# Kernel optimization log

Measured on AMD Instinct MI355X. Metric: run time of the kernel, lower is better.

## Reference

```python
import jax, jax.numpy as jnp
import numpy as np

H = 400      # LSTM hidden units
K = 10       # attention window mixture components (mixtures=30 -> alpha/beta/kappa of size K)
V = 61       # vocab_size
NOUT = 121   # MDN head: 1 eos + 20*(pi, mu1, mu2, sigma1, sigma2, rho)


def setup_inputs():
    key = jax.random.key(0)
    ks = jax.random.split(key, 12)
    B, T, U = 32, 600, 64
    s = 0.05
    d = {}
    d['strokes'] = jax.random.normal(ks[0], (B, T, 3), jnp.float32)
    d['sentence'] = jax.random.uniform(ks[1], (B, U, V), dtype=jnp.float32)
    d['W1'] = jax.random.normal(ks[2], (3 + V, 4 * H), jnp.float32) * s
    d['U1r'] = jax.random.normal(ks[3], (H, 4 * H), jnp.float32) * s
    d['b1'] = jnp.zeros((4 * H,), jnp.float32)
    d['Ww'] = jax.random.normal(ks[4], (H, 3 * K), jnp.float32) * s
    d['bw'] = jnp.zeros((3 * K,), jnp.float32)
    d['W2'] = jax.random.normal(ks[5], (3 + V + H, 4 * H), jnp.float32) * s
    d['U2r'] = jax.random.normal(ks[6], (H, 4 * H), jnp.float32) * s
    d['b2'] = jnp.zeros((4 * H,), jnp.float32)
    d['W3'] = jax.random.normal(ks[7], (3 + V + H, 4 * H), jnp.float32) * s
    d['U3r'] = jax.random.normal(ks[8], (H, 4 * H), jnp.float32) * s
    d['b3'] = jnp.zeros((4 * H,), jnp.float32)
    d['Wm'] = jax.random.normal(ks[9], (3 * H, NOUT), jnp.float32) * s
    d['bm'] = jnp.zeros((NOUT,), jnp.float32)
    return d


def _lstm(x_tbd, W, Ur, b, h0, c0):
    # standard Keras-order (i, f, g, o) LSTM over time-major input [T,B,D]
    def step(carry, xt):
        h, c = carry
        z = xt @ W + h @ Ur + b
        i, f, g, o = jnp.split(z, 4, axis=-1)
        c = jax.nn.sigmoid(f) * c + jax.nn.sigmoid(i) * jnp.tanh(g)
        h = jax.nn.sigmoid(o) * jnp.tanh(c)
        return (h, c), h
    _, hs = jax.lax.scan(step, (h0, c0), x_tbd)
    return hs


def _forward(strokes, sentence, W1, U1r, b1, Ww, bw, W2, U2r, b2, W3, U3r, b3, Wm, bm):
    B, T, _ = strokes.shape
    U = sentence.shape[1]
    u_grid = jnp.arange(U, dtype=strokes.dtype)           # character positions
    x_tb = jnp.transpose(strokes, (1, 0, 2))               # [T,B,3]
    h0 = jnp.zeros((B, H), strokes.dtype)
    w0 = jnp.zeros((B, V), strokes.dtype)
    k0 = jnp.zeros((B, K), strokes.dtype)

    def step1(carry, xt):
        # Graves synthesis windowed LSTM cell: LSTM on [x_t, w_{t-1}],
        # then Gaussian-mixture soft attention over the sentence.
        h, c, w, kappa = carry
        xin = jnp.concatenate([xt, w], axis=-1)            # [B, 3+V]
        z = xin @ W1 + h @ U1r + b1
        i, f, g, o = jnp.split(z, 4, axis=-1)
        c = jax.nn.sigmoid(f) * c + jax.nn.sigmoid(i) * jnp.tanh(g)
        h = jax.nn.sigmoid(o) * jnp.tanh(c)
        p = h @ Ww + bw                                    # [B, 3K]
        alpha = jnp.exp(p[:, :K])
        beta = jnp.exp(p[:, K:2 * K])
        kappa = kappa + jnp.exp(p[:, 2 * K:])
        # phi(u) = sum_k alpha_k exp(-beta_k (kappa_k - u)^2)  -> [B,U]
        phi = jnp.einsum('bk,bku->bu', alpha,
                         jnp.exp(-beta[:, :, None] * (kappa[:, :, None] - u_grid) ** 2))
        w = jnp.einsum('bu,buv->bv', phi, sentence)        # soft window [B,V]
        return (h, c, w, kappa), jnp.concatenate([h, w], axis=-1)

    _, o1 = jax.lax.scan(step1, (h0, h0, w0, k0), x_tb)    # [T,B,H+V]
    lstm1 = o1[:, :, :H]
    win = o1[:, :, H:]
    in2 = jnp.concatenate([x_tb, win, lstm1], axis=-1)     # skip1: [T,B,3+V+H]
    lstm2 = _lstm(in2, W2, U2r, b2, h0, h0)
    in3 = jnp.concatenate([x_tb, win, lstm2], axis=-1)     # skip2
    lstm3 = _lstm(in3, W3, U3r, b3, h0, h0)
    y = jnp.concatenate([lstm1, lstm2, lstm3], axis=-1) @ Wm + bm  # [T,B,121]
    # MDN mixture coefficients
    e = jax.nn.sigmoid(y[..., 0:1])
    pi = jax.nn.softmax(y[..., 1:21], axis=-1)
    mu1 = y[..., 21:41]
    mu2 = y[..., 41:61]
    s1 = jnp.exp(y[..., 61:81])
    s2 = jnp.exp(y[..., 81:101])
    rho = jnp.tanh(y[..., 101:121])
    out = jnp.concatenate([e, pi, mu1, mu2, s1, s2, rho], axis=-1)
    return jnp.transpose(out, (1, 0, 2))                   # [B,T,121]


def reference(strokes, sentence, W1, U1r, b1, Ww, bw, W2, U2r, b2, W3, U3r, b3, Wm, bm):
    return _forward(strokes, sentence, W1, U1r, b1, Ww, bw, W2, U2r, b2, W3, U3r, b3, Wm, bm)
```

## Files before the change

kernel.cpp:

```cpp
#include <hip/hip_runtime.h>
#include <math.h>

#define T 600
#define NBLK 235

#define SEN1 256
#define SEN2 1536
#define SEN3 3072
#define SENB 4608

#define OFF_UT1 8192
#define SZ_UT1 (1600*480)
#define OFF_UT2 (OFF_UT1 + SZ_UT1)
#define SZ_UT2 (1600*960)
#define OFF_UT3 (OFF_UT2 + SZ_UT2)
#define OFF_WWT (OFF_UT3 + SZ_UT2)
#define SZ_WWT (30*400)
#define OFF_H1 (OFF_WWT + SZ_WWT)
#define SZ_H (600*32*400)
#define OFF_H2 (OFF_H1 + SZ_H)
#define OFF_H3 (OFF_H2 + SZ_H)
#define OFF_W  (OFF_H3 + SZ_H)
#define SZ_W (600*32*61)

#define LDS_W    0
#define LDS_V    19280
#define LDS_Z    34640
#define LDS_C    35408
#define LDS_TOT  35600

__device__ __forceinline__ float sigm(float x) { return 1.f/(1.f+expf(-x)); }

#define WBAR() do { \
    asm volatile("s_waitcnt lgkmcnt(0)" ::: "memory"); \
    __builtin_amdgcn_sched_barrier(0); \
} while (0)

__global__ void init_ws(unsigned* uws) {
    for (int i = threadIdx.x + blockIdx.x*blockDim.x; i < 8192; i += blockDim.x*gridDim.x)
        uws[i] = 0u;
}

__global__ void build_ut(float* __restrict__ ws,
                         const float* __restrict__ W1, const float* __restrict__ U1r,
                         const float* __restrict__ W2, const float* __restrict__ U2r,
                         const float* __restrict__ W3, const float* __restrict__ U3r,
                         const float* __restrict__ Ww) {
    const long N1 = 1600L*480, N2 = 1600L*960;
    const long total = N1 + 2*N2 + 30L*400;
    for (long i = blockIdx.x*(long)blockDim.x + threadIdx.x; i < total;
         i += (long)gridDim.x*blockDim.x) {
        if (i < N1) {
            long c = i / 480, k = i % 480;
            float v = 0.f;
            if (k < 64) v = W1[k*1600 + c];
            else if (k < 464) v = U1r[(k-64)*1600 + c];
            ws[OFF_UT1 + c*480 + k] = v;
        } else if (i < N1 + N2) {
            long ii = i - N1; long c = ii/960, k = ii%960;
            float v = 0.f;
            if (k < 464) v = W2[k*1600 + c];
            else if (k >= 480 && k < 880) v = U2r[(k-480)*1600 + c];
            ws[OFF_UT2 + c*960 + k] = v;
        } else if (i < N1 + 2*N2) {
            long ii = i - N1 - N2; long c = ii/960, k = ii%960;
            float v = 0.f;
            if (k < 464) v = W3[k*1600 + c];
            else if (k >= 480 && k < 880) v = U3r[(k-480)*1600 + c];
            ws[OFF_UT3 + c*960 + k] = v;
        } else {
            long ii = i - N1 - 2*N2; long n = ii/400, k = ii%400;
            ws[OFF_WWT + n*400 + k] = Ww[k*30 + n];
        }
    }
}

__device__ __forceinline__ unsigned ld_cohere(const unsigned* p) {
    unsigned v;
    asm volatile("global_load_dword %0, %1, off sc0 sc1\n\t"
                 "s_waitcnt vmcnt(0)"
                 : "=v"(v) : "v"(p) : "memory");
    return v;
}
__device__ __forceinline__ void st_wt(float* p, float v) {
    asm volatile("global_store_dword %0, %1, off sc0 sc1\n\t"
                 "s_waitcnt vmcnt(0)"
                 :: "v"(p), "v"(v) : "memory");
}
__device__ __forceinline__ void st_wt_u(unsigned* p, unsigned v) {
    asm volatile("global_store_dword %0, %1, off sc0 sc1\n\t"
                 "s_waitcnt vmcnt(0)"
                 :: "v"(p), "v"(v) : "memory");
}
__device__ __forceinline__ void wait_sen(const unsigned* sen, int count,
                                         unsigned tgt, int tid) {
    if (tid < 64) {
        for (;;) {
            unsigned m = 0xFFFFFFFFu;
            for (int i = tid; i < count; i += 64) {
                unsigned v = ld_cohere(sen + (size_t)i*16);
                m = (v < m) ? v : m;
            }
            if (__all(m >= tgt)) break;
            __builtin_amdgcn_s_sleep(1);
        }
    }
    __syncthreads();
}

template<int NQ, int KCN, int K4S, int LO, int HI>
__device__ __forceinline__ void gemm_pass(const float4* __restrict__ w4,
                                          const float4* __restrict__ v4,
                                          int lc0, int kc, int bq, int kofs4,
                                          float acc[8][4]) {
    #pragma unroll
    for (int q = 0; q < NQ; ++q) {
        int kfv = q*KCN + kc;
        if (kfv >= LO && kfv < HI) {
            int xv = kfv ^ ((kfv >> 3) & 7);
            int kfw = kofs4 + kfv;
            int xw = kfw ^ ((kfw >> 3) & 7);
            float4 va[8];
            #pragma unroll
            for (int i = 0; i < 8; ++i) va[i] = v4[(bq*8+i)*120 + xv];
            #pragma unroll
            for (int j = 0; j < 4; ++j) {
                float4 u = w4[(lc0+j)*K4S + xw];
                #pragma unroll
                for (int i = 0; i < 8; ++i)
                    acc[i][j] += va[i].x*u.x + va[i].y*u.y + va[i].z*u.z + va[i].w*u.w;
            }
        }
    }
}

__launch_bounds__(512)
__global__ void hw_main(float* __restrict__ ws,
                        const float* __restrict__ strokes, const float* __restrict__ sentence,
                        const float* __restrict__ b1, const float* __restrict__ b2,
                        const float* __restrict__ b3, const float* __restrict__ bw) {
    extern __shared__ float S[];
    const int tid = threadIdx.x;
    const int bid = blockIdx.x;
    unsigned* uws = (unsigned*)ws;
    const unsigned* sen1 = uws + SEN1;
    const unsigned* sen2 = uws + SEN2;
    const unsigned* sen3 = uws + SEN3;
    const unsigned* senB = uws + SENB;

    int role, unit0 = 0, nu = 0, L = 0, b0a = 0;
    const float* utp = nullptr; const float* biasp = nullptr; float* hout = nullptr;
    if (bid < 67)       { role = 0; L = bid;      unit0 = L*6; nu = (bid==66)?4:6; utp = ws+OFF_UT1; biasp = b1; hout = ws+OFF_H1; }
    else if (bid < 147) { role = 1; L = bid-67;   unit0 = L*5; nu = 5;             utp = ws+OFF_UT2; biasp = b2; hout = ws+OFF_H2; }
    else if (bid < 227) { role = 2; L = bid-147;  unit0 = L*5; nu = 5;             utp = ws+OFF_UT3; biasp = b3; hout = ws+OFF_H3; }
    else                { role = 3; L = bid-227;  b0a = L*4; }

    if (role <= 2) {
        const int NC = 4*nu;
        const int KCN = (role == 0) ? 20 : 24;
        const int K4S = (role == 0) ? 121 : 241;
        const int K4TOT = (role == 0) ? 120 : 240;
        const int uts = (role == 0) ? 480 : 960;
        float4* w4 = (float4*)S;
        float4* v4 = (float4*)(S + LDS_V);
        float*  vf = S + LDS_V;
        float*  z_lds = S + LDS_Z;
        float*  c_lds = S + LDS_C;

        for (int idx = tid; idx < NC*K4TOT; idx += 512) {
            int colL = idx / K4TOT, kf = idx % K4TOT;
            int gcol = (colL/nu)*400 + unit0 + (colL%nu);
            float4 val = *(const float4*)(utp + (size_t)gcol*uts + kf*4);
            w4[colL*K4S + (kf ^ ((kf>>3)&7))] = val;
        }
        for (int i = tid; i < 192; i += 512) c_lds[i] = 0.f;

        const int tile = tid / KCN, kc = tid % KCN;
        const int bq = tile / nu, cq = tile % nu;
        const bool act = (tile < 4*nu);
        float bias0 = 0.f, bias1 = 0.f;
        if (tid < 32*NC)       { int lc = tid % NC;        bias0 = biasp[(lc/nu)*400 + unit0 + (lc%nu)]; }
        if (tid + 512 < 32*NC) { int lc = (tid+512) % NC;  bias1 = biasp[(lc/nu)*400 + unit0 + (lc%nu)]; }
        const int nrole = (role == 0) ? 67 : 80;
        const unsigned* mysen = (role == 0) ? sen1 : ((role == 1) ? sen2 : sen3);
        unsigned* myword = (unsigned*)mysen + (size_t)L*16;
        __syncthreads();

        for (int t = 0; t < T; ++t) {
            float acc[8][4];
            #pragma unroll
            for (int i = 0; i < 8; ++i)
                #pragma unroll
                for (int j = 0; j < 4; ++j) acc[i][j] = 0.f;

            if (role == 0) {
                if (t > 0) wait_sen(sen1, 67, (unsigned)t, tid);
                const float* hsrc = (t > 0) ? (ws + OFF_H1 + (size_t)(t-1)*12800) : nullptr;
                for (int idx = tid; idx < 32*104; idx += 512) {
                    int b = idx/104, kf = 16 + idx%104;
                    float4 val = {0.f,0.f,0.f,0.f};
                    if (kf < 116 && hsrc) val = *(const float4*)(hsrc + b*400 + (kf*4 - 64));
                    v4[b*120 + (kf ^ ((kf>>3)&7))] = val;
                }
                __syncthreads();
                if (act) gemm_pass<6,20,121,16,116>(w4, v4, cq*4, kc, bq, 0, acc);
                if (t > 0) wait_sen(senB, 8, (unsigned)t, tid);
                const float* wsrc = (t > 0) ? (ws + OFF_W + (size_t)(t-1)*1952) : nullptr;
                {
                    int b = tid / 16, kf = tid % 16;
                    if (b < 32) {
                        float4 val;
                        if (kf == 0) {
                            const float* xp = strokes + ((size_t)b*600 + t)*3;
                            val.x = xp[0]; val.y = xp[1]; val.z = xp[2];
                            val.w = wsrc ? wsrc[b*61] : 0.f;
                        } else {
                            int k0 = kf*4 - 3;
                            if (wsrc) { val.x = wsrc[b*61+k0]; val.y = wsrc[b*61+k0+1];
                                        val.z = wsrc[b*61+k0+2]; val.w = wsrc[b*61+k0+3]; }
                            else { val.x=val.y=val.z=val.w=0.f; }
                        }
                        v4[b*120 + (kf ^ ((kf>>3)&7))] = val;
                    }
                }
                __syncthreads();
                if (act) gemm_pass<6,20,121,0,16>(w4, v4, cq*4, kc, bq, 0, acc);
            } else {
                if (role == 1) wait_sen(sen1, 67, (unsigned)(t+1), tid);
                else           wait_sen(sen2, 80, (unsigned)(t+1), tid);
                const float* hsrc = ws + ((role==1)?OFF_H1:OFF_H2) + (size_t)t*12800;
                for (int idx = tid; idx < 32*104; idx += 512) {
                    int b = idx/104, kf = 16 + idx%104;
                    float4 val = {0.f,0.f,0.f,0.f};
                    if (kf < 116) val = *(const float4*)(hsrc + b*400 + (kf*4 - 64));
                    v4[b*120 + (kf ^ ((kf>>3)&7))] = val;
                }
                __syncthreads();
                if (act) gemm_pass<5,24,241,16,116>(w4, v4, cq*4, kc, bq, 0, acc);
                wait_sen(senB, 8, (unsigned)(t+1), tid);
                const float* wsrc = ws + OFF_W + (size_t)t*1952;
                {
                    int b = tid / 16, kf = tid % 16;
                    if (b < 32) {
                        float4 val;
                        if (kf == 0) {
                            const float* xp = strokes + ((size_t)b*600 + t)*3;
                            val.x = xp[0]; val.y = xp[1]; val.z = xp[2];
                            val.w = wsrc[b*61];
                        } else {
                            int k0 = kf*4 - 3;
                            val.x = wsrc[b*61+k0]; val.y = wsrc[b*61+k0+1];
                            val.z = wsrc[b*61+k0+2]; val.w = wsrc[b*61+k0+3];
                        }
                        v4[b*120 + (kf ^ ((kf>>3)&7))] = val;
                    }
                }
                __syncthreads();
                if (act) gemm_pass<5,24,241,0,16>(w4, v4, cq*4, kc, bq, 0, acc);
                __syncthreads();
                if (t > 0) wait_sen(mysen, nrole, (unsigned)t, tid);
                const float* hp2 = (t > 0) ? (ws + ((role==1)?OFF_H2:OFF_H3) + (size_t)(t-1)*12800) : nullptr;
                for (int idx = tid; idx < 32*120; idx += 512) {
                    int b = idx/120, kf = idx%120;
                    float4 val = {0.f,0.f,0.f,0.f};
                    if (kf < 100 && hp2) val = *(const float4*)(hp2 + b*400 + kf*4);
                    v4[b*120 + (kf ^ ((kf>>3)&7))] = val;
                }
                __syncthreads();
                if (act) gemm_pass<5,24,241,0,100>(w4, v4, cq*4, kc, bq, 120, acc);
            }

            __syncthreads();
            const int halfk = (KCN+1)/2;
            const int SCRW = NC*32 + 4;
            const int NO = 32*NC;
            if (act && kc < halfk) {
                #pragma unroll
                for (int i = 0; i < 8; ++i) {
                    float4 w;
                    w.x=acc[i][0]; w.y=acc[i][1]; w.z=acc[i][2]; w.w=acc[i][3];
                    *(float4*)&vf[kc*SCRW + (bq*8+i)*NC + cq*4] = w;
                }
            }
            __syncthreads();
            float zs0 = 0.f, zs1 = 0.f;
            if (tid < NO)       for (int k2 = 0; k2 < halfk; ++k2) zs0 += vf[k2*SCRW + tid];
            if (tid + 512 < NO) for (int k2 = 0; k2 < halfk; ++k2) zs1 += vf[k2*SCRW + tid + 512];
            __syncthreads();
            if (act && kc >= halfk) {
                #pragma unroll
                for (int i = 0; i < 8; ++i) {
                    float4 w;
                    w.x=acc[i][0]; w.y=acc[i][1]; w.z=acc[i][2]; w.w=acc[i][3];
                    *(float4*)&vf[(kc-halfk)*SCRW + (bq*8+i)*NC + cq*4] = w;
                }
            }
            __syncthreads();
            const int rem = KCN - halfk;
            if (tid < NO) {
                for (int k2 = 0; k2 < rem; ++k2) zs0 += vf[k2*SCRW + tid];
                z_lds[tid] = zs0 + bias0;
            }
            if (tid + 512 < NO) {
                for (int k2 = 0; k2 < rem; ++k2) zs1 += vf[k2*SCRW + tid + 512];
                z_lds[tid + 512] = zs1 + bias1;
            }
            __syncthreads();
            if (tid < 32*nu) {
                int b = tid & 31, ju = tid >> 5;
                float zi = z_lds[b*NC + ju];
                float zf = z_lds[b*NC + nu + ju];
                float zg = z_lds[b*NC + 2*nu + ju];
                float zo = z_lds[b*NC + 3*nu + ju];
                float cP = c_lds[b*6 + ju];
                float cN = sigm(zf)*cP + sigm(zi)*tanhf(zg);
                float hN = sigm(zo)*tanhf(cN);
                c_lds[b*6 + ju] = cN;
                st_wt(&hout[(size_t)t*12800 + b*400 + unit0 + ju], hN);
            }
            __syncthreads();
            if (tid == 0) st_wt_u(myword, (unsigned)(t+1));
        }
    } else {
        const int wv = tid >> 6, lane = tid & 63;
        float* hb   = S;
        float* pb   = S + 1600 + (tid>>6)*32;
        float* ab   = S + 1792 + (tid>>6)*32;
        float* kap  = S + 1984 + (tid>>6)*16;
        float* phiW = S + 2112 + (tid>>6)*64;
        float* sentl= S + 2368;
        float* wwt  = S + 2368 + 15616;
        float* hbW  = hb + wv*400;
        float4* hb4 = (float4*)hbW;
        unsigned* myword = (unsigned*)senB + (size_t)L*16;

        for (int i = tid; i < 64; i += 512) (S + 1984)[i] = 0.f;
        for (int i = tid; i < 15616; i += 512) sentl[i] = sentence[(size_t)b0a*3904 + i];
        for (int i = tid; i < 12000; i += 512) {
            int n = i/400, k = i%400;
            wwt[n*404 + k] = ws[OFF_WWT + i];
        }
        float bwv = (lane < 60 && !(lane & 1)) ? bw[lane >> 1] : 0.f;
        __syncthreads();

        for (int t = 0; t < T; ++t) {
            wait_sen(sen1, 67, (unsigned)(t+1), tid);
            if (wv < 4) {
                const float* h1t = ws + OFF_H1 + (size_t)t*12800 + (size_t)(b0a+wv)*400;
                for (int i = lane; i < 100; i += 64)
                    hb4[i] = *(const float4*)(h1t + i*4);
                WBAR();
                if (lane < 60) {
                    int n = lane >> 1, hf = lane & 1;
                    const float4* ww4 = (const float4*)(wwt + n*404) + hf*50;
                    const float4* hh4 = hb4 + hf*50;
                    float a = 0.f;
                    #pragma unroll 5
                    for (int i = 0; i < 50; ++i) {
                        float4 h = hh4[i], w = ww4[i];
                        a += h.x*w.x + h.y*w.y + h.z*w.z + h.w*w.w;
                    }
                    a += __shfl_xor(a, 1);
                    if (hf == 0) pb[n] = a + bwv;
                }
                WBAR();
                if (lane < 10) {
                    ab[lane]      = expf(pb[lane]);
                    ab[16 + lane] = expf(pb[10 + lane]);
                    kap[lane]    += expf(pb[20 + lane]);
                }
                WBAR();
                {
                    float uf = (float)lane, ph = 0.f;
                    #pragma unroll
                    for (int k0 = 0; k0 < 10; ++k0) {
                        float d = kap[k0] - uf;
                        ph += ab[k0]*expf(-ab[16 + k0]*d*d);
                    }
                    phiW[lane] = ph;
                }
                WBAR();
                if (lane < 61) {
                    const float* sp = sentl + wv*3904 + lane;
                    float wvv = 0.f;
                    #pragma unroll 4
                    for (int u = 0; u < 64; ++u) wvv += phiW[u]*sp[u*61];
                    st_wt(&ws[OFF_W + (size_t)t*1952 + (size_t)(b0a+wv)*61 + lane], wvv);
                }
            }
            __syncthreads();
            if (tid == 0) st_wt_u(myword, (unsigned)(t+1));
        }
    }
}

__launch_bounds__(256)
__global__ void out_proj(const float* __restrict__ ws, const float* __restrict__ Wm,
                         const float* __restrict__ bm, float* __restrict__ out) {
    __shared__ __align__(16) float hc[8*1200];
    __shared__ float yy[8*121];
    __shared__ float sm2[16];
    const int tid = threadIdx.x;
    const long rowbase = (long)blockIdx.x * 8;
    const float* h1h = ws + OFF_H1;
    const float* h2h = ws + OFF_H2;
    const float* h3h = ws + OFF_H3;
    for (int idx = tid; idx < 8*1200; idx += 256) {
        int i = idx/1200, k = idx%1200;
        long r = rowbase + i; int t = (int)(r >> 5), b = (int)(r & 31);
        float v;
        if (k < 400)      v = h1h[(size_t)t*12800 + b*400 + k];
        else if (k < 800) v = h2h[(size_t)t*12800 + b*400 + (k-400)];
        else              v = h3h[(size_t)t*12800 + b*400 + (k-800)];
        hc[i*1200 + k] = v;
    }
    __syncthreads();
    const int j = tid & 127, rr = tid >> 7;
    if (j < 121) {
        float a0=0.f, a1=0.f, a2=0.f, a3=0.f;
        const float* r0 = &hc[(rr*4+0)*1200];
        const float* r1 = &hc[(rr*4+1)*1200];
        const float* r2 = &hc[(rr*4+2)*1200];
        const float* r3 = &hc[(rr*4+3)*1200];
        for (int k = 0; k < 1200; ++k) {
            float wm = Wm[(size_t)k*121 + j];
            a0 += r0[k]*wm; a1 += r1[k]*wm; a2 += r2[k]*wm; a3 += r3[k]*wm;
        }
        float bb = bm[j];
        yy[(rr*4+0)*121 + j] = a0 + bb;
        yy[(rr*4+1)*121 + j] = a1 + bb;
        yy[(rr*4+2)*121 + j] = a2 + bb;
        yy[(rr*4+3)*121 + j] = a3 + bb;
    }
    __syncthreads();
    if (tid < 8) {
        const float* yr = &yy[tid*121];
        float m = yr[1];
        for (int q = 2; q < 21; ++q) m = fmaxf(m, yr[q]);
        float ssum = 0.f;
        for (int q = 1; q < 21; ++q) ssum += expf(yr[q] - m);
        sm2[tid*2] = m; sm2[tid*2+1] = ssum;
    }
    __syncthreads();
    if (j < 121) {
        for (int i2 = 0; i2 < 4; ++i2) {
            int i = rr*4 + i2;
            long r = rowbase + i; int t = (int)(r >> 5), b = (int)(r & 31);
            float y = yy[i*121 + j], o;
            if (j == 0)      o = 1.f/(1.f + expf(-y));
            else if (j < 21) o = expf(y - sm2[i*2]) / sm2[i*2+1];
            else if (j < 61) o = y;
            else if (j < 101) o = expf(y);
            else             o = tanhf(y);
            out[((size_t)b*600 + t)*121 + j] = o;
        }
    }
}

extern "C" void kernel_launch(void* const* d_in, const int* in_sizes, int n_in,
                              void* d_out, int out_size, void* d_ws, size_t ws_size,
                              hipStream_t stream) {
    const float* strokes  = (const float*)d_in[0];
    const float* sentence = (const float*)d_in[1];
    const float* W1  = (const float*)d_in[2];
    const float* U1r = (const float*)d_in[3];
    const float* b1  = (const float*)d_in[4];
    const float* Ww  = (const float*)d_in[5];
    const float* bw  = (const float*)d_in[6];
    const float* W2  = (const float*)d_in[7];
    const float* U2r = (const float*)d_in[8];
    const float* b2  = (const float*)d_in[9];
    const float* W3  = (const float*)d_in[10];
    const float* U3r = (const float*)d_in[11];
    const float* b3  = (const float*)d_in[12];
    const float* Wm  = (const float*)d_in[13];
    const float* bm  = (const float*)d_in[14];
    float* ws = (float*)d_ws;
    float* out = (float*)d_out;

    const int dyn_bytes = LDS_TOT * 4;
    (void)hipFuncSetAttribute((const void*)hw_main,
                              hipFuncAttributeMaxDynamicSharedMemorySize, dyn_bytes);

    init_ws<<<dim3(4), dim3(512), 0, stream>>>((unsigned*)ws);
    build_ut<<<dim3(1024), dim3(256), 0, stream>>>(ws, W1, U1r, W2, U2r, W3, U3r, Ww);
    hw_main<<<dim3(NBLK), dim3(512), dyn_bytes, stream>>>(ws, strokes, sentence, b1, b2, b3, bw);
    out_proj<<<dim3(2400), dim3(256), 0, stream>>>(ws, Wm, bm, out);
}
```

Measured before the change: 10.43 ms.

## Precompute sentence-projected weights and replicate attention window per block

Precomputes sentence×W_window products per block's gate columns in a new build kernel, so the window contribution to each LSTM gate becomes phi·(S W) instead of first forming w then multiplying by W. Removes the dedicated attention blocks and their barrier: every LSTM block recomputes the attention (kappa, phi) redundantly from h1 and applies it directly, cutting one cross-block dependency per timestep. It also changes the k-split from 20/24 to 16 lanes and replaces the LDS reduction with shuffle reductions. The costs are redundant attention work in all 227 blocks, extra workspace, and a phi threshold skip that slightly changes the numerics.

```diff
diff --git a/kernel.cpp b/kernel.cpp
--- a/kernel.cpp
+++ b/kernel.cpp
@@ -2,12 +2,11 @@
 #include <math.h>
 
 #define T 600
-#define NBLK 235
+#define NBLK 227
 
 #define SEN1 256
 #define SEN2 1536
 #define SEN3 3072
-#define SENB 4608
 
 #define OFF_UT1 8192
 #define SZ_UT1 (1600*480)
@@ -20,21 +19,23 @@
 #define SZ_H (600*32*400)
 #define OFF_H2 (OFF_H1 + SZ_H)
 #define OFF_H3 (OFF_H2 + SZ_H)
-#define OFF_W  (OFF_H3 + SZ_H)
-#define SZ_W (600*32*61)
+#define OFF_SW1 (OFF_H3 + SZ_H)
+#define SZ_SW1 (67*32*64*24)
+#define OFF_SW2 (OFF_SW1 + SZ_SW1)
+#define SZ_SW2 (80*32*64*20)
+#define OFF_SW3 (OFF_SW2 + SZ_SW2)
 
 #define LDS_W    0
 #define LDS_V    19280
 #define LDS_Z    34640
 #define LDS_C    35408
-#define LDS_TOT  35600
+#define LDS_KAP  35600
+#define LDS_PB   35920
+#define LDS_AB   36880
+#define LDS_PHI  37520
+#define LDS_TOT  39568
 
 __device__ __forceinline__ float sigm(float x) { return 1.f/(1.f+expf(-x)); }
-
-#define WBAR() do { \
-    asm volatile("s_waitcnt lgkmcnt(0)" ::: "memory"); \
-    __builtin_amdgcn_sched_barrier(0); \
-} while (0)
 
 __global__ void init_ws(unsigned* uws) {
     for (int i = threadIdx.x + blockIdx.x*blockDim.x; i < 8192; i += blockDim.x*gridDim.x)
@@ -75,6 +76,49 @@
     }
 }
 
+__global__ void build_sw(float* __restrict__ ws, const float* __restrict__ sentence,
+                         const float* __restrict__ W1, const float* __restrict__ W2,
+                         const float* __restrict__ W3) {
+    const long N1 = 67L*49152, N2 = 80L*40960;
+    const long total = N1 + 2*N2;
+    for (long o = blockIdx.x*(long)blockDim.x + threadIdx.x; o < total;
+         o += (long)gridDim.x*blockDim.x) {
+        float acc = 0.f;
+        long dst;
+        if (o < N1) {
+            long L = o / 49152, r = o % 49152;
+            long b = r / 1536, r2 = r % 1536, u = r2 / 24, lc = r2 % 24;
+            int nu = (L == 66) ? 4 : 6;
+            dst = OFF_SW1 + o;
+            if (lc < 4*nu) {
+                int gcol = (int)((lc/nu)*400 + L*6 + (lc%nu));
+                const float* sp = sentence + ((size_t)b*64 + u)*61;
+                for (int v = 0; v < 61; ++v)
+                    acc += sp[v] * W1[(size_t)(3+v)*1600 + gcol];
+            }
+        } else if (o < N1 + N2) {
+            long oo = o - N1;
+            long L = oo / 40960, r = oo % 40960;
+            long b = r / 1280, r2 = r % 1280, u = r2 / 20, lc = r2 % 20;
+            dst = OFF_SW2 + oo;
+            int gcol = (int)((lc/5)*400 + L*5 + (lc%5));
+            const float* sp = sentence + ((size_t)b*64 + u)*61;
+            for (int v = 0; v < 61; ++v)
+                acc += sp[v] * W2[(size_t)(3+v)*1600 + gcol];
+        } else {
+            long oo = o - N1 - N2;
+            long L = oo / 40960, r = oo % 40960;
+            long b = r / 1280, r2 = r % 1280, u = r2 / 20, lc = r2 % 20;
+            dst = OFF_SW3 + oo;
+            int gcol = (int)((lc/5)*400 + L*5 + (lc%5));
+            const float* sp = sentence + ((size_t)b*64 + u)*61;
+            for (int v = 0; v < 61; ++v)
+                acc += sp[v] * W3[(size_t)(3+v)*1600 + gcol];
+        }
+        ws[dst] = acc;
+    }
+}
+
 __device__ __forceinline__ unsigned ld_cohere(const unsigned* p) {
     unsigned v;
     asm volatile("global_load_dword %0, %1, off sc0 sc1\n\t"
@@ -104,6 +148,46 @@
             if (__all(m >= tgt)) break;
             __builtin_amdgcn_s_sleep(1);
         }
+    }
+    __syncthreads();
+}
+
+__device__ __forceinline__ void attn_phase(int tid, const float4* __restrict__ v4,
+                                           const float* __restrict__ wwt, float bw_reg,
+                                           float* pbuf, float* ab, float* kap, float* phi) {
+    if (tid < 480) {
+        int n = tid % 30, g = tid / 30;
+        int bA = g*2, bB = bA + 1;
+        const float4* wt4 = (const float4*)wwt + n*100;
+        float a0 = 0.f, a1 = 0.f;
+        #pragma unroll 4
+        for (int kfi = 0; kfi < 100; ++kfi) {
+            int kf = kfi + 16, xv = kf ^ ((kf>>3)&7);
+            float4 wv = wt4[kfi];
+            float4 hA = v4[bA*120 + xv], hB = v4[bB*120 + xv];
+            a0 += hA.x*wv.x + hA.y*wv.y + hA.z*wv.z + hA.w*wv.w;
+            a1 += hB.x*wv.x + hB.y*wv.y + hB.z*wv.z + hB.w*wv.w;
+        }
+        pbuf[bA*30 + n] = a0 + bw_reg;
+        pbuf[bB*30 + n] = a1 + bw_reg;
+    }
+    __syncthreads();
+    if (tid < 320) {
+        int b = tid/10, k = tid%10;
+        ab[b*20 + k]      = expf(pbuf[b*30 + k]);
+        ab[b*20 + 10 + k] = expf(pbuf[b*30 + 10 + k]);
+        kap[b*10 + k]    += expf(pbuf[b*30 + 20 + k]);
+    }
+    __syncthreads();
+    for (int o = tid; o < 2048; o += 512) {
+        int b = o >> 6, u = o & 63;
+        float uf = (float)u, ph = 0.f;
+        #pragma unroll
+        for (int k = 0; k < 10; ++k) {
+            float d = kap[b*10 + k] - uf;
+            ph += ab[b*20 + k]*expf(-ab[b*20 + 10 + k]*d*d);
+        }
+        phi[o] = ph;
     }
     __syncthreads();
 }
@@ -136,7 +220,7 @@
 
 __launch_bounds__(512)
 __global__ void hw_main(float* __restrict__ ws,
-                        const float* __restrict__ strokes, const float* __restrict__ sentence,
+                        const float* __restrict__ strokes,
                         const float* __restrict__ b1, const float* __restrict__ b2,
                         const float* __restrict__ b3, const float* __restrict__ bw) {
     extern __shared__ float S[];
@@ -146,251 +230,190 @@
     const unsigned* sen1 = uws + SEN1;
     const unsigned* sen2 = uws + SEN2;
     const unsigned* sen3 = uws + SEN3;
-    const unsigned* senB = uws + SENB;
-
-    int role, unit0 = 0, nu = 0, L = 0, b0a = 0;
-    const float* utp = nullptr; const float* biasp = nullptr; float* hout = nullptr;
+
+    int role, unit0, nu, L;
+    const float* utp; const float* biasp; float* hout;
     if (bid < 67)       { role = 0; L = bid;      unit0 = L*6; nu = (bid==66)?4:6; utp = ws+OFF_UT1; biasp = b1; hout = ws+OFF_H1; }
     else if (bid < 147) { role = 1; L = bid-67;   unit0 = L*5; nu = 5;             utp = ws+OFF_UT2; biasp = b2; hout = ws+OFF_H2; }
-    else if (bid < 227) { role = 2; L = bid-147;  unit0 = L*5; nu = 5;             utp = ws+OFF_UT3; biasp = b3; hout = ws+OFF_H3; }
-    else                { role = 3; L = bid-227;  b0a = L*4; }
-
-    if (role <= 2) {
-        const int NC = 4*nu;
-        const int KCN = (role == 0) ? 20 : 24;
-        const int K4S = (role == 0) ? 121 : 241;
-        const int K4TOT = (role == 0) ? 120 : 240;
-        const int uts = (role == 0) ? 480 : 960;
-        float4* w4 = (float4*)S;
-        float4* v4 = (float4*)(S + LDS_V);
-        float*  vf = S + LDS_V;
-        float*  z_lds = S + LDS_Z;
-        float*  c_lds = S + LDS_C;
-
-        for (int idx = tid; idx < NC*K4TOT; idx += 512) {
-            int colL = idx / K4TOT, kf = idx % K4TOT;
-            int gcol = (colL/nu)*400 + unit0 + (colL%nu);
-            float4 val = *(const float4*)(utp + (size_t)gcol*uts + kf*4);
-            w4[colL*K4S + (kf ^ ((kf>>3)&7))] = val;
-        }
-        for (int i = tid; i < 192; i += 512) c_lds[i] = 0.f;
-
-        const int tile = tid / KCN, kc = tid % KCN;
-        const int bq = tile / nu, cq = tile % nu;
-        const bool act = (tile < 4*nu);
-        float bias0 = 0.f, bias1 = 0.f;
-        if (tid < 32*NC)       { int lc = tid % NC;        bias0 = biasp[(lc/nu)*400 + unit0 + (lc%nu)]; }
-        if (tid + 512 < 32*NC) { int lc = (tid+512) % NC;  bias1 = biasp[(lc/nu)*400 + unit0 + (lc%nu)]; }
-        const int nrole = (role == 0) ? 67 : 80;
-        const unsigned* mysen = (role == 0) ? sen1 : ((role == 1) ? sen2 : sen3);
-        unsigned* myword = (unsigned*)mysen + (size_t)L*16;
+    else                { role = 2; L = bid-147;  unit0 = L*5; nu = 5;             utp = ws+OFF_UT3; biasp = b3; hout = ws+OFF_H3; }
+
+    const int NC = 4*nu;
+    const int K4S = (role == 0) ? 121 : 241;
+    const int K4TOT = (role == 0) ? 120 : 240;
+    const int uts = (role == 0) ? 480 : 960;
+    float4* w4 = (float4*)S;
+    float4* v4 = (float4*)(S + LDS_V);
+    float*  z_lds = S + LDS_Z;
+    float*  c_lds = S + LDS_C;
+    float*  kap   = S + LDS_KAP;
+    float*  pb    = S + LDS_PB;
+    float*  ab    = S + LDS_AB;
+    float*  phi   = S + LDS_PHI;
+    const float* wwt = ws + OFF_WWT;
+
+    for (int idx = tid; idx < NC*K4TOT; idx += 512) {
+        int colL = idx / K4TOT, kf = idx % K4TOT;
+        int gcol = (colL/nu)*400 + unit0 + (colL%nu);
+        float4 val = *(const float4*)(utp + (size_t)gcol*uts + kf*4);
+        w4[colL*K4S + (kf ^ ((kf>>3)&7))] = val;
+    }
+    for (int i = tid; i < 192; i += 512) c_lds[i] = 0.f;
+    for (int i = tid; i < 320; i += 512) kap[i] = 0.f;
+
+    const int tile = tid >> 4, kc = tid & 15;
+    const int bq = tile / nu, cq = tile % nu;
+    const bool act = (tile < 4*nu);
+    const float bw_reg = (tid < 480) ? bw[tid % 30] : 0.f;
+    float bI = 0.f, bF = 0.f, bG = 0.f, bO = 0.f;
+    if (tid < 32*nu) {
+        int ju = tid >> 5;
+        bI = biasp[unit0 + ju];        bF = biasp[400 + unit0 + ju];
+        bG = biasp[800 + unit0 + ju];  bO = biasp[1200 + unit0 + ju];
+    }
+    const unsigned* mysen = (role == 0) ? sen1 : ((role == 1) ? sen2 : sen3);
+    unsigned* myword = (unsigned*)mysen + (size_t)L*16;
+    const float* swbase; int NCP;
+    if (role == 0)      { swbase = ws + OFF_SW1 + (size_t)L*49152; NCP = 24; }
+    else if (role == 1) { swbase = ws + OFF_SW2 + (size_t)L*40960; NCP = 20; }
+    else                { swbase = ws + OFF_SW3 + (size_t)L*40960; NCP = 20; }
+    __syncthreads();
+
+    for (int t = 0; t < T; ++t) {
+        float acc[8][4];
+        #pragma unroll
+        for (int i = 0; i < 8; ++i)
+            #pragma unroll
+            for (int j = 0; j < 4; ++j) acc[i][j] = 0.f;
+
+        if (role == 0) {
+            if (t > 0) wait_sen(sen1, 67, (unsigned)t, tid);
+            const float* hsrc = (t > 0) ? (ws + OFF_H1 + (size_t)(t-1)*12800) : nullptr;
+            for (int idx = tid; idx < 3200; idx += 512) {
+                int b = idx/100, kfi = idx%100, kf = 16 + kfi;
+                float4 val = {0.f,0.f,0.f,0.f};
+                if (hsrc) val = *(const float4*)(hsrc + b*400 + kfi*4);
+                v4[b*120 + (kf ^ ((kf>>3)&7))] = val;
+            }
+            {
+                int b = tid >> 4, kf = tid & 15;
+                float4 val = {0.f,0.f,0.f,0.f};
+                if (kf == 0) {
+                    const float* xp = strokes + ((size_t)b*600 + t)*3;
+                    val.x = xp[0]; val.y = xp[1]; val.z = xp[2];
+                }
+                v4[b*120 + (kf ^ ((kf>>3)&7))] = val;
+            }
+            __syncthreads();
+            if (t > 0) {
+                attn_phase(tid, v4, wwt, bw_reg, pb, ab, kap, phi);
+                for (int o = tid; o < 32*NC; o += 512) {
+                    int b = o / NC, lc = o - b*NC;
+                    const float* swp = swbase + ((size_t)b*64)*NCP + lc;
+                    const float* php = phi + (size_t)b*64;
+                    float a = 0.f;
+                    for (int u = 0; u < 64; ++u) {
+                        float pv = php[u];
+                        if (pv > 1e-8f) a += pv * swp[(size_t)u*NCP];
+                    }
+                    pb[o] = a;
+                }
+            } else {
+                for (int o = tid; o < 32*NC; o += 512) pb[o] = 0.f;
+            }
+            __syncthreads();
+            if (act) {
+                gemm_pass<8,16,121,0,1>(w4, v4, cq*4, kc, bq, 0, acc);
+                gemm_pass<8,16,121,16,116>(w4, v4, cq*4, kc, bq, 0, acc);
+            }
+        } else {
+            if (role == 1) wait_sen(sen1, 67, (unsigned)(t+1), tid);
+            else           wait_sen(sen2, 80, (unsigned)(t+1), tid);
+            const float* h1t = ws + OFF_H1 + (size_t)t*12800;
+            for (int idx = tid; idx < 3200; idx += 512) {
+                int b = idx/100, kfi = idx%100, kf = 16 + kfi;
+                v4[b*120 + (kf ^ ((kf>>3)&7))] = *(const float4*)(h1t + b*400 + kfi*4);
+            }
+            __syncthreads();
+            attn_phase(tid, v4, wwt, bw_reg, pb, ab, kap, phi);
+            for (int o = tid; o < 32*NC; o += 512) {
+                int b = o / NC, lc = o - b*NC;
+                const float* swp = swbase + ((size_t)b*64)*NCP + lc;
+                const float* php = phi + (size_t)b*64;
+                float a = 0.f;
+                for (int u = 0; u < 64; ++u) {
+                    float pv = php[u];
+                    if (pv > 1e-8f) a += pv * swp[(size_t)u*NCP];
+                }
+                pb[o] = a;
+            }
+            __syncthreads();
+            if (role == 2) {
+                const float* h2t = ws + OFF_H2 + (size_t)t*12800;
+                for (int idx = tid; idx < 3200; idx += 512) {
+                    int b = idx/100, kfi = idx%100, kf = 16 + kfi;
+                    v4[b*120 + (kf ^ ((kf>>3)&7))] = *(const float4*)(h2t + b*400 + kfi*4);
+                }
+            }
+            {
+                int b = tid >> 4, kf = tid & 15;
+                float4 val = {0.f,0.f,0.f,0.f};
+                if (kf == 0) {
+                    const float* xp = strokes + ((size_t)b*600 + t)*3;
+                    val.x = xp[0]; val.y = xp[1]; val.z = xp[2];
+                }
+                v4[b*120 + (kf ^ ((kf>>3)&7))] = val;
+            }
+            __syncthreads();
+            if (act) {
+                gemm_pass<8,16,241,0,1>(w4, v4, cq*4, kc, bq, 0, acc);
+                gemm_pass<8,16,241,16,116>(w4, v4, cq*4, kc, bq, 0, acc);
+            }
+            if (t > 0) wait_sen(mysen, 80, (unsigned)t, tid);
+            else       __syncthreads();
+            const float* hp2 = (t > 0) ? (ws + ((role==1)?OFF_H2:OFF_H3) + (size_t)(t-1)*12800) : nullptr;
+            for (int idx = tid; idx < 3840; idx += 512) {
+                int b = idx/120, kf = idx%120;
+                float4 val = {0.f,0.f,0.f,0.f};
+                if (kf < 100 && hp2) val = *(const float4*)(hp2 + b*400 + kf*4);
+                v4[b*120 + (kf ^ ((kf>>3)&7))] = val;
+            }
+            __syncthreads();
+            if (act) gemm_pass<7,16,241,0,100>(w4, v4, cq*4, kc, bq, 120, acc);
+        }
+
+        if (act) {
+            #pragma unroll
+            for (int m = 1; m < 16; m <<= 1)
+                #pragma unroll
+                for (int i = 0; i < 8; ++i)
+                    #pragma unroll
+                    for (int j = 0; j < 4; ++j)
+                        acc[i][j] += __shfl_xor(acc[i][j], m, 64);
+            float o0 = 0.f, o1 = 0.f;
+            #pragma unroll
+            for (int i = 0; i < 4; ++i)
+                #pragma unroll
+                for (int j = 0; j < 4; ++j)
+                    if (kc == i*4+j) { o0 = acc[i][j]; o1 = acc[i+4][j]; }
+            int i0 = kc >> 2, j0 = kc & 3;
+            z_lds[(bq*8 + i0)*NC + cq*4 + j0] = o0;
+            z_lds[(bq*8 + 4 + i0)*NC + cq*4 + j0] = o1;
+        }
         __syncthreads();
-
-        for (int t = 0; t < T; ++t) {
-            float acc[8][4];
-            #pragma unroll
-            for (int i = 0; i < 8; ++i)
-                #pragma unroll
-                for (int j = 0; j < 4; ++j) acc[i][j] = 0.f;
-
-            if (role == 0) {
-                if (t > 0) wait_sen(sen1, 67, (unsigned)t, tid);
-                const float* hsrc = (t > 0) ? (ws + OFF_H1 + (size_t)(t-1)*12800) : nullptr;
-                for (int idx = tid; idx < 32*104; idx += 512) {
-                    int b = idx/104, kf = 16 + idx%104;
-                    float4 val = {0.f,0.f,0.f,0.f};
-                    if (kf < 116 && hsrc) val = *(const float4*)(hsrc + b*400 + (kf*4 - 64));
-                    v4[b*120 + (kf ^ ((kf>>3)&7))] = val;
-                }
-                __syncthreads();
-                if (act) gemm_pass<6,20,121,16,116>(w4, v4, cq*4, kc, bq, 0, acc);
-                if (t > 0) wait_sen(senB, 8, (unsigned)t, tid);
-                const float* wsrc = (t > 0) ? (ws + OFF_W + (size_t)(t-1)*1952) : nullptr;
-                {
-                    int b = tid / 16, kf = tid % 16;
-                    if (b < 32) {
-                        float4 val;
-                        if (kf == 0) {
-                            const float* xp = strokes + ((size_t)b*600 + t)*3;
-                            val.x = xp[0]; val.y = xp[1]; val.z = xp[2];
-                            val.w = wsrc ? wsrc[b*61] : 0.f;
-                        } else {
-                            int k0 = kf*4 - 3;
-                            if (wsrc) { val.x = wsrc[b*61+k0]; val.y = wsrc[b*61+k0+1];
-                                        val.z = wsrc[b*61+k0+2]; val.w = wsrc[b*61+k0+3]; }
-                            else { val.x=val.y=val.z=val.w=0.f; }
-                        }
-                        v4[b*120 + (kf ^ ((kf>>3)&7))] = val;
-                    }
-                }
-                __syncthreads();
-                if (act) gemm_pass<6,20,121,0,16>(w4, v4, cq*4, kc, bq, 0, acc);
-            } else {
-                if (role == 1) wait_sen(sen1, 67, (unsigned)(t+1), tid);
-                else           wait_sen(sen2, 80, (unsigned)(t+1), tid);
-                const float* hsrc = ws + ((role==1)?OFF_H1:OFF_H2) + (size_t)t*12800;
-                for (int idx = tid; idx < 32*104; idx += 512) {
-                    int b = idx/104, kf = 16 + idx%104;
-                    float4 val = {0.f,0.f,0.f,0.f};
-                    if (kf < 116) val = *(const float4*)(hsrc + b*400 + (kf*4 - 64));
-                    v4[b*120 + (kf ^ ((kf>>3)&7))] = val;
-                }
-                __syncthreads();
-                if (act) gemm_pass<5,24,241,16,116>(w4, v4, cq*4, kc, bq, 0, acc);
-                wait_sen(senB, 8, (unsigned)(t+1), tid);
-                const float* wsrc = ws + OFF_W + (size_t)t*1952;
-                {
-                    int b = tid / 16, kf = tid % 16;
-                    if (b < 32) {
-                        float4 val;
-                        if (kf == 0) {
-                            const float* xp = strokes + ((size_t)b*600 + t)*3;
-                            val.x = xp[0]; val.y = xp[1]; val.z = xp[2];
-                            val.w = wsrc[b*61];
-                        } else {
-                            int k0 = kf*4 - 3;
-                            val.x = wsrc[b*61+k0]; val.y = wsrc[b*61+k0+1];
-                            val.z = wsrc[b*61+k0+2]; val.w = wsrc[b*61+k0+3];
-                        }
-                        v4[b*120 + (kf ^ ((kf>>3)&7))] = val;
-                    }
-                }
-                __syncthreads();
-                if (act) gemm_pass<5,24,241,0,16>(w4, v4, cq*4, kc, bq, 0, acc);
-                __syncthreads();
-                if (t > 0) wait_sen(mysen, nrole, (unsigned)t, tid);
-                const float* hp2 = (t > 0) ? (ws + ((role==1)?OFF_H2:OFF_H3) + (size_t)(t-1)*12800) : nullptr;
-                for (int idx = tid; idx < 32*120; idx += 512) {
-                    int b = idx/120, kf = idx%120;
-                    float4 val = {0.f,0.f,0.f,0.f};
-                    if (kf < 100 && hp2) val = *(const float4*)(hp2 + b*400 + kf*4);
-                    v4[b*120 + (kf ^ ((kf>>3)&7))] = val;
-                }
-                __syncthreads();
-                if (act) gemm_pass<5,24,241,0,100>(w4, v4, cq*4, kc, bq, 120, acc);
-            }
-
-            __syncthreads();
-            const int halfk = (KCN+1)/2;
-            const int SCRW = NC*32 + 4;
-            const int NO = 32*NC;
-            if (act && kc < halfk) {
-                #pragma unroll
-                for (int i = 0; i < 8; ++i) {
-                    float4 w;
-                    w.x=acc[i][0]; w.y=acc[i][1]; w.z=acc[i][2]; w.w=acc[i][3];
-                    *(float4*)&vf[kc*SCRW + (bq*8+i)*NC + cq*4] = w;
-                }
-            }
-            __syncthreads();
-            float zs0 = 0.f, zs1 = 0.f;
-            if (tid < NO)       for (int k2 = 0; k2 < halfk; ++k2) zs0 += vf[k2*SCRW + tid];
-            if (tid + 512 < NO) for (int k2 = 0; k2 < halfk; ++k2) zs1 += vf[k2*SCRW + tid + 512];
-            __syncthreads();
-            if (act && kc >= halfk) {
-                #pragma unroll
-                for (int i = 0; i < 8; ++i) {
-                    float4 w;
-                    w.x=acc[i][0]; w.y=acc[i][1]; w.z=acc[i][2]; w.w=acc[i][3];
-                    *(float4*)&vf[(kc-halfk)*SCRW + (bq*8+i)*NC + cq*4] = w;
-                }
-            }
-            __syncthreads();
-            const int rem = KCN - halfk;
-            if (tid < NO) {
-                for (int k2 = 0; k2 < rem; ++k2) zs0 += vf[k2*SCRW + tid];
-                z_lds[tid] = zs0 + bias0;
-            }
-            if (tid + 512 < NO) {
-                for (int k2 = 0; k2 < rem; ++k2) zs1 += vf[k2*SCRW + tid + 512];
-                z_lds[tid + 512] = zs1 + bias1;
-            }
-            __syncthreads();
-            if (tid < 32*nu) {
-                int b = tid & 31, ju = tid >> 5;
-                float zi = z_lds[b*NC + ju];
-                float zf = z_lds[b*NC + nu + ju];
-                float zg = z_lds[b*NC + 2*nu + ju];
-                float zo = z_lds[b*NC + 3*nu + ju];
-                float cP = c_lds[b*6 + ju];
-                float cN = sigm(zf)*cP + sigm(zi)*tanhf(zg);
-                float hN = sigm(zo)*tanhf(cN);
-                c_lds[b*6 + ju] = cN;
-                st_wt(&hout[(size_t)t*12800 + b*400 + unit0 + ju], hN);
-            }
-            __syncthreads();
-            if (tid == 0) st_wt_u(myword, (unsigned)(t+1));
-        }
-    } else {
-        const int wv = tid >> 6, lane = tid & 63;
-        float* hb   = S;
-        float* pb   = S + 1600 + (tid>>6)*32;
-        float* ab   = S + 1792 + (tid>>6)*32;
-        float* kap  = S + 1984 + (tid>>6)*16;
-        float* phiW = S + 2112 + (tid>>6)*64;
-        float* sentl= S + 2368;
-        float* wwt  = S + 2368 + 15616;
-        float* hbW  = hb + wv*400;
-        float4* hb4 = (float4*)hbW;
-        unsigned* myword = (unsigned*)senB + (size_t)L*16;
-
-        for (int i = tid; i < 64; i += 512) (S + 1984)[i] = 0.f;
-        for (int i = tid; i < 15616; i += 512) sentl[i] = sentence[(size_t)b0a*3904 + i];
-        for (int i = tid; i < 12000; i += 512) {
-            int n = i/400, k = i%400;
-            wwt[n*404 + k] = ws[OFF_WWT + i];
-        }
-        float bwv = (lane < 60 && !(lane & 1)) ? bw[lane >> 1] : 0.f;
+        if (tid < 32*nu) {
+            int b = tid & 31, ju = tid >> 5;
+            float zi = z_lds[b*NC + ju]        + pb[b*NC + ju]        + bI;
+            float zf = z_lds[b*NC + nu + ju]   + pb[b*NC + nu + ju]   + bF;
+            float zg = z_lds[b*NC + 2*nu + ju] + pb[b*NC + 2*nu + ju] + bG;
+            float zo = z_lds[b*NC + 3*nu + ju] + pb[b*NC + 3*nu + ju] + bO;
+            float cP = c_lds[b*6 + ju];
+            float cN = sigm(zf)*cP + sigm(zi)*tanhf(zg);
+            float hN = sigm(zo)*tanhf(cN);
+            c_lds[b*6 + ju] = cN;
+            st_wt(&hout[(size_t)t*12800 + b*400 + unit0 + ju], hN);
+        }
         __syncthreads();
-
-        for (int t = 0; t < T; ++t) {
-            wait_sen(sen1, 67, (unsigned)(t+1), tid);
-            if (wv < 4) {
-                const float* h1t = ws + OFF_H1 + (size_t)t*12800 + (size_t)(b0a+wv)*400;
-                for (int i = lane; i < 100; i += 64)
-                    hb4[i] = *(const float4*)(h1t + i*4);
-                WBAR();
-                if (lane < 60) {
-                    int n = lane >> 1, hf = lane & 1;
-                    const float4* ww4 = (const float4*)(wwt + n*404) + hf*50;
-                    const float4* hh4 = hb4 + hf*50;
-                    float a = 0.f;
-                    #pragma unroll 5
-                    for (int i = 0; i < 50; ++i) {
-                        float4 h = hh4[i], w = ww4[i];
-                        a += h.x*w.x + h.y*w.y + h.z*w.z + h.w*w.w;
-                    }
-                    a += __shfl_xor(a, 1);
-                    if (hf == 0) pb[n] = a + bwv;
-                }
-                WBAR();
-                if (lane < 10) {
-                    ab[lane]      = expf(pb[lane]);
-                    ab[16 + lane] = expf(pb[10 + lane]);
-                    kap[lane]    += expf(pb[20 + lane]);
-                }
-                WBAR();
-                {
-                    float uf = (float)lane, ph = 0.f;
-                    #pragma unroll
-                    for (int k0 = 0; k0 < 10; ++k0) {
-                        float d = kap[k0] - uf;
-                        ph += ab[k0]*expf(-ab[16 + k0]*d*d);
-                    }
-                    phiW[lane] = ph;
-                }
-                WBAR();
-                if (lane < 61) {
-                    const float* sp = sentl + wv*3904 + lane;
-                    float wvv = 0.f;
-                    #pragma unroll 4
-                    for (int u = 0; u < 64; ++u) wvv += phiW[u]*sp[u*61];
-                    st_wt(&ws[OFF_W + (size_t)t*1952 + (size_t)(b0a+wv)*61 + lane], wvv);
-                }
-            }
-            __syncthreads();
-            if (tid == 0) st_wt_u(myword, (unsigned)(t+1));
-        }
+        if (tid == 0) st_wt_u(myword, (unsigned)(t+1));
     }
 }
 
@@ -484,6 +507,7 @@
 
     init_ws<<<dim3(4), dim3(512), 0, stream>>>((unsigned*)ws);
     build_ut<<<dim3(1024), dim3(256), 0, stream>>>(ws, W1, U1r, W2, U2r, W3, U3r, Ww);
-    hw_main<<<dim3(NBLK), dim3(512), dyn_bytes, stream>>>(ws, strokes, sentence, b1, b2, b3, bw);
+    build_sw<<<dim3(4096), dim3(256), 0, stream>>>(ws, sentence, W1, W2, W3);
+    hw_main<<<dim3(NBLK), dim3(512), dyn_bytes, stream>>>(ws, strokes, b1, b2, b3, bw);
     out_proj<<<dim3(2400), dim3(256), 0, stream>>>(ws, Wm, bm, out);
 }
```

New measurement: 28.33 ms. +171.6%, slower.

## Pack sentinel flags densely and merge layer-2/3 input staging into one wait

Applied to the files above, without the earlier changes.

Sentinel counters for each role move from one per 64-byte line to densely packed consecutive words, so a polling wave reads fewer cache lines per check. Layers 2 and 3 now stage the stroke/window input and the lower-layer h in a single loop and run one GEMM pass over k 0..116 instead of two. Layer 2 waits only on the attention-window sentinel, on the assumption that the window being ready implies layer 1's h is ready. Packing the flags risks false sharing between writers that store to the same cache line.

```diff
diff --git a/kernel.cpp b/kernel.cpp
--- a/kernel.cpp
+++ b/kernel.cpp
@@ -5,9 +5,9 @@
 #define NBLK 235
 
 #define SEN1 256
-#define SEN2 1536
-#define SEN3 3072
-#define SENB 4608
+#define SEN2 384
+#define SEN3 512
+#define SENB 640
 
 #define OFF_UT1 8192
 #define SZ_UT1 (1600*480)
@@ -98,7 +98,7 @@
         for (;;) {
             unsigned m = 0xFFFFFFFFu;
             for (int i = tid; i < count; i += 64) {
-                unsigned v = ld_cohere(sen + (size_t)i*16);
+                unsigned v = ld_cohere(sen + i);
                 m = (v < m) ? v : m;
             }
             if (__all(m >= tgt)) break;
@@ -183,7 +183,7 @@
         if (tid + 512 < 32*NC) { int lc = (tid+512) % NC;  bias1 = biasp[(lc/nu)*400 + unit0 + (lc%nu)]; }
         const int nrole = (role == 0) ? 67 : 80;
         const unsigned* mysen = (role == 0) ? sen1 : ((role == 1) ? sen2 : sen3);
-        unsigned* myword = (unsigned*)mysen + (size_t)L*16;
+        unsigned* myword = (unsigned*)mysen + L;
         __syncthreads();
 
         for (int t = 0; t < T; ++t) {
@@ -196,7 +196,7 @@
             if (role == 0) {
                 if (t > 0) wait_sen(sen1, 67, (unsigned)t, tid);
                 const float* hsrc = (t > 0) ? (ws + OFF_H1 + (size_t)(t-1)*12800) : nullptr;
-                for (int idx = tid; idx < 32*104; idx += 512) {
+                for (int idx = tid; idx < 3328; idx += 512) {
                     int b = idx/104, kf = 16 + idx%104;
                     float4 val = {0.f,0.f,0.f,0.f};
                     if (kf < 116 && hsrc) val = *(const float4*)(hsrc + b*400 + (kf*4 - 64));
@@ -226,41 +226,33 @@
                 __syncthreads();
                 if (act) gemm_pass<6,20,121,0,16>(w4, v4, cq*4, kc, bq, 0, acc);
             } else {
-                if (role == 1) wait_sen(sen1, 67, (unsigned)(t+1), tid);
+                if (role == 1) wait_sen(senB, 8, (unsigned)(t+1), tid);
                 else           wait_sen(sen2, 80, (unsigned)(t+1), tid);
                 const float* hsrc = ws + ((role==1)?OFF_H1:OFF_H2) + (size_t)t*12800;
-                for (int idx = tid; idx < 32*104; idx += 512) {
-                    int b = idx/104, kf = 16 + idx%104;
-                    float4 val = {0.f,0.f,0.f,0.f};
-                    if (kf < 116) val = *(const float4*)(hsrc + b*400 + (kf*4 - 64));
+                const float* wsrc = ws + OFF_W + (size_t)t*1952;
+                for (int idx = tid; idx < 3840; idx += 512) {
+                    int b = idx/120, kf = idx%120;
+                    float4 val;
+                    if (kf >= 16) {
+                        if (kf < 116) val = *(const float4*)(hsrc + b*400 + (kf*4 - 64));
+                        else { val.x=val.y=val.z=val.w=0.f; }
+                    } else if (kf == 0) {
+                        const float* xp = strokes + ((size_t)b*600 + t)*3;
+                        val.x = xp[0]; val.y = xp[1]; val.z = xp[2];
+                        val.w = wsrc[b*61];
+                    } else {
+                        int k0 = kf*4 - 3;
+                        val.x = wsrc[b*61+k0]; val.y = wsrc[b*61+k0+1];
+                        val.z = wsrc[b*61+k0+2]; val.w = wsrc[b*61+k0+3];
+                    }
                     v4[b*120 + (kf ^ ((kf>>3)&7))] = val;
                 }
                 __syncthreads();
-                if (act) gemm_pass<5,24,241,16,116>(w4, v4, cq*4, kc, bq, 0, acc);
-                wait_sen(senB, 8, (unsigned)(t+1), tid);
-                const float* wsrc = ws + OFF_W + (size_t)t*1952;
-                {
-                    int b = tid / 16, kf = tid % 16;
-                    if (b < 32) {
-                        float4 val;
-                        if (kf == 0) {
-                            const float* xp = strokes + ((size_t)b*600 + t)*3;
-                            val.x = xp[0]; val.y = xp[1]; val.z = xp[2];
-                            val.w = wsrc[b*61];
-                        } else {
-                            int k0 = kf*4 - 3;
-                            val.x = wsrc[b*61+k0]; val.y = wsrc[b*61+k0+1];
-                            val.z = wsrc[b*61+k0+2]; val.w = wsrc[b*61+k0+3];
-                        }
-                        v4[b*120 + (kf ^ ((kf>>3)&7))] = val;
-                    }
-                }
+                if (act) gemm_pass<5,24,241,0,116>(w4, v4, cq*4, kc, bq, 0, acc);
                 __syncthreads();
-                if (act) gemm_pass<5,24,241,0,16>(w4, v4, cq*4, kc, bq, 0, acc);
-                __syncthreads();
-                if (t > 0) wait_sen(mysen, nrole, (unsigned)t, tid);
+                if (t > 0) wait_sen(mysen, 80, (unsigned)t, tid);
                 const float* hp2 = (t > 0) ? (ws + ((role==1)?OFF_H2:OFF_H3) + (size_t)(t-1)*12800) : nullptr;
-                for (int idx = tid; idx < 32*120; idx += 512) {
+                for (int idx = tid; idx < 3840; idx += 512) {
                     int b = idx/120, kf = idx%120;
                     float4 val = {0.f,0.f,0.f,0.f};
                     if (kf < 100 && hp2) val = *(const float4*)(hp2 + b*400 + kf*4);
@@ -332,7 +324,7 @@
         float* wwt  = S + 2368 + 15616;
         float* hbW  = hb + wv*400;
         float4* hb4 = (float4*)hbW;
-        unsigned* myword = (unsigned*)senB + (size_t)L*16;
+        unsigned* myword = (unsigned*)senB + L;
 
         for (int i = tid; i < 64; i += 512) (S + 1984)[i] = 0.f;
         for (int i = tid; i < 15616; i += 512) sentl[i] = sentence[(size_t)b0a*3904 + i];
```

Result: no change. 10.51 ms (+0.8%).
